# Optimization experiments

Measured on AMD Instinct MI355X. Metric: run time of the kernel, lower is better.

The kernel has to match this reference:

```python
import jax, jax.numpy as jnp
import numpy as np

BIT = 64
N_DATA = 200000
TOP_FNPS = 20
THRESHOLD = 0.3
K = 2500
T = 0.9 * float(np.sqrt(BIT))
MOMENTUM = 0.4
HIGH = int(N_DATA * 0.9)
BATCH = 256


def _l2norm(x):
    return x / jnp.linalg.norm(x, axis=-1, keepdims=True)


def setup_inputs() -> dict:
    key = jax.random.key(0)
    ks = jax.random.split(key, 7)
    i_A = jax.random.normal(ks[0], (BATCH, BIT), jnp.float32)
    i_B = jax.random.normal(ks[1], (BATCH, BIT), jnp.float32)
    t_A = jax.random.normal(ks[2], (BATCH, BIT), jnp.float32)
    t_B = jax.random.normal(ks[3], (BATCH, BIT), jnp.float32)
    # memory bank: F.normalize(sign(randn)) -> rows are +-1/sqrt(bit)
    memory = jnp.sign(jax.random.normal(ks[4], (N_DATA, BIT), jnp.float32)) / np.float32(np.sqrt(BIT))
    # uniform keys used for randperm-equivalent negative sampling (top-K of random keys)
    rand_u = jax.random.uniform(ks[5], (BATCH, N_DATA), jnp.float32)
    batch_idx = jax.random.randint(ks[6], (BATCH,), 0, N_DATA)
    return {"i_A": i_A, "i_B": i_B, "t_A": t_A, "t_B": t_B,
            "memory": memory, "rand_u": rand_u, "batch_idx": batch_idx}


def reference(i_A, i_B, t_A, t_B, memory, rand_u, batch_idx):
    f1 = (i_A + t_A) * 0.5  # anchor fusion [B, bit]
    f2 = (i_A + t_B) * 0.5
    f3 = (i_B + t_A) * 0.5
    f4 = (i_B + t_B) * 0.5
    # sim_k = memory @ norm(f_k).T ; final_sim = mean of 4 (mm is linear in the fusion)
    fsum = (_l2norm(f1) + _l2norm(f2) + _l2norm(f3) + _l2norm(f4)) * 0.25
    final_sim = fsum @ memory.T  # [B, N]

    def per_sample(sim_col, ru, pos, anchor):
        # sim_col: [N], ru: [N] uniform keys, pos: scalar idx, anchor: [bit]
        topv, topi = jax.lax.top_k(sim_col, TOP_FNPS)
        fnp_valid = (topv > THRESHOLD) & (topi != pos)  # false-negative pairs mask
        excl = jnp.zeros((N_DATA,), bool).at[topi].set(fnp_valid).at[pos].set(True)
        # candidates = top HIGH entries of descending sort == sims >= HIGH-th largest value
        kth = jnp.sort(sim_col)[N_DATA - HIGH]
        cand = (sim_col >= kth) & (~excl)
        keys = jnp.where(cand, ru, -jnp.inf)
        _, neg_idx = jax.lax.top_k(keys, K)  # uniform K-subset of candidates
        pos_s = jnp.sign(memory[pos])          # [bit]
        fnp_s = jnp.sign(memory[topi])         # [TOP_FNPS, bit]
        neg_s = jnp.sign(memory[neg_idx])      # [K, bit]
        pos_sim = jnp.dot(pos_s, anchor) / T
        fnp_sim = (fnp_s @ anchor) / T
        neg_sim = (neg_s @ anchor) / T
        vmask = fnp_valid.astype(anchor.dtype)
        pos_exp = jnp.exp(pos_sim)
        # numerator = pos_exp + sum(beta * fnp_exp), beta = fnp_sim
        numerator = pos_exp + jnp.sum(fnp_sim * jnp.exp(fnp_sim) * vmask)
        denominator = jnp.sum(jnp.exp(neg_sim)) + pos_exp
        n_fnp = jnp.sum(vmask)
        return -jnp.log(numerator / denominator) / (1.0 + n_fnp)

    losses = jax.vmap(per_sample)(final_sim, rand_u, batch_idx, f1)
    avg_loss = jnp.mean(losses)

    # momentum memory-bank update (torch.no_grad block)
    new_feature = _l2norm(f1)
    old_feature = memory[batch_idx] * MOMENTUM + new_feature * (1.0 - MOMENTUM)
    old_feature = _l2norm(old_feature)
    new_memory = memory.at[batch_idx].set(old_feature)
    return avg_loss, new_memory
```

## Files before the change

kernel.cpp:

```cpp
#include <hip/hip_runtime.h>
#include <stdint.h>

#define NDATA 200000
#define BATCH 256
#define BITD  64
#define TOPF  20
#define KNEG  2500
#define RANKA 20000
#define TVAL  7.2f
#define S8T   (8.0f/7.2f)
#define THRV  0.3f
#define TAU   0.983f
#define KHINV 60235.294f

#define NB    512
#define HCUT  320
#define HLO   (-0.35f)
#define HINV  1024.0f

#define CFX   2048
#define CNX3  4096
#define NCHK  200
#define CAPN  44
#define CAPF  36
#define WCH   8
#define BLKF  512
#define HSLC  8

typedef unsigned long long u64;
typedef __attribute__((ext_vector_type(16))) float f32x16;
typedef __attribute__((ext_vector_type(8))) short s16x8;

__device__ __forceinline__ int binOf(float sim) {
    int b = (int)floorf((sim - HLO) * HINV);
    b = b < 0 ? 0 : b;
    b = b > (NB - 1) ? (NB - 1) : b;
    return b;
}
__device__ __forceinline__ unsigned short bf16_rne(float x) {
    unsigned u = __float_as_uint(x);
    unsigned r = (u + 0x7FFFu + ((u >> 16) & 1u)) >> 16;
    return (unsigned short)r;
}
__device__ __forceinline__ float bf2f(unsigned short u) {
    return __uint_as_float(((unsigned)u) << 16);
}

__global__ __launch_bounds__(64) void k_prep(
    const float* __restrict__ iA, const float* __restrict__ iB,
    const float* __restrict__ tA, const float* __restrict__ tB,
    const float* __restrict__ mem, const int* __restrict__ bidx,
    unsigned short* __restrict__ fsumHi, unsigned short* __restrict__ fsumLo,
    float* __restrict__ fsumF, float* __restrict__ f1_g,
    float* __restrict__ upd_g, float* __restrict__ posExp_g,
    unsigned* __restrict__ hist_gp,
    unsigned* __restrict__ negBaseG, unsigned* __restrict__ fnpBaseG)
{
    int s = blockIdx.x, j = threadIdx.x;
    float a = iA[s * BITD + j], b = iB[s * BITD + j];
    float c = tA[s * BITD + j], d = tB[s * BITD + j];
    float f1 = 0.5f * (a + c), f2 = 0.5f * (a + d);
    float f3 = 0.5f * (b + c), f4 = 0.5f * (b + d);
    float q1 = f1 * f1, q2 = f2 * f2, q3 = f3 * f3, q4 = f4 * f4;
#pragma unroll
    for (int m = 1; m < 64; m <<= 1) {
        q1 += __shfl_xor(q1, m); q2 += __shfl_xor(q2, m);
        q3 += __shfl_xor(q3, m); q4 += __shfl_xor(q4, m);
    }
    float n1 = sqrtf(q1), n2 = sqrtf(q2), n3 = sqrtf(q3), n4 = sqrtf(q4);
    float fs = 0.25f * (f1 / n1 + f2 / n2 + f3 / n3 + f4 / n4);

    unsigned short hi = bf16_rne(fs);
    float hif = __uint_as_float(((unsigned)hi) << 16);
    unsigned short lo = bf16_rne(fs - hif);
    fsumHi[s * BITD + j] = hi;
    fsumLo[s * BITD + j] = lo;
    fsumF[s * BITD + j] = fs;
    f1_g[s * BITD + j] = f1;

    int pos = bidx[s];
    float mv = mem[(size_t)pos * BITD + j];
    float sg = (mv > 0.f) ? 1.f : ((mv < 0.f) ? -1.f : 0.f);
    float ps = sg * f1;
#pragma unroll
    for (int m = 1; m < 64; m <<= 1) ps += __shfl_xor(ps, m);

    float nf = f1 / n1;
    float u = mv * 0.4f + nf * 0.6f;
    float uq = u * u;
#pragma unroll
    for (int m = 1; m < 64; m <<= 1) uq += __shfl_xor(uq, m);
    upd_g[s * BITD + j] = u / sqrtf(uq);

    if (j == 0) {
        posExp_g[s] = expf(ps / TVAL);
        negBaseG[s] = 0u; fnpBaseG[s] = 0u;
    }
    int gtid = s * 64 + j;
    for (int k = gtid; k < HSLC * (BATCH / 2) * HCUT; k += BATCH * 64) hist_gp[k] = 0u;
}

__global__ __launch_bounds__(256) void k_pack(const float* __restrict__ mem,
                                              unsigned short* __restrict__ memB,
                                              float* __restrict__ out)
{
    int t2 = blockIdx.x;
    int t = threadIdx.x;
    int sl = t & 31, h = (t >> 5) & 1, ks = t >> 6;
    int row = t2 * 32 + sl;
    int col = ks * 16 + 8 * h;
    const float* src = mem + (size_t)row * BITD + col;
    float4 v0 = *(const float4*)src;
    float4 v1 = *(const float4*)(src + 4);
    s16x8 o;
    o[0] = (short)bf16_rne(v0.x); o[1] = (short)bf16_rne(v0.y);
    o[2] = (short)bf16_rne(v0.z); o[3] = (short)bf16_rne(v0.w);
    o[4] = (short)bf16_rne(v1.x); o[5] = (short)bf16_rne(v1.y);
    o[6] = (short)bf16_rne(v1.z); o[7] = (short)bf16_rne(v1.w);
    *(s16x8*)(memB + ((size_t)(t2 * 4 + ks) * 2 + h) * 256 + sl * 8) = o;
    float* dst = out + 1 + (size_t)row * BITD + col;
    dst[0] = v0.x; dst[1] = v0.y; dst[2] = v0.z; dst[3] = v0.w;
    dst[4] = v1.x; dst[5] = v1.y; dst[6] = v1.z; dst[7] = v1.w;
}

__global__ __launch_bounds__(256, 4) void k_main(
    const unsigned short* __restrict__ memB, const float* __restrict__ ru,
    const unsigned short* __restrict__ fsumHi, const unsigned short* __restrict__ fsumLo,
    const float* __restrict__ f1_g, const float* __restrict__ fsumF,
    unsigned* __restrict__ negPayC, u64* __restrict__ fnpPayC,
    unsigned* __restrict__ negBaseG, unsigned* __restrict__ fnpBaseG,
    unsigned* __restrict__ hist_gp)
{
    __shared__ unsigned histL[8 * HCUT];
    __shared__ unsigned negPayL[32 * CAPN * 3];
    __shared__ u64 fnpPayL[32 * CAPF];
    __shared__ unsigned negCntL[32], fnpCntL[32];
    __shared__ unsigned negBaseL[32], fnpBaseL[32];

    const int tid = threadIdx.x;
    const int w = tid >> 6, l = tid & 63;
    const int h = l >> 5, sl = l & 31;

    const int bid = blockIdx.x;
    const int chunk = (bid & 7) + 8 * (bid >> 6);
    const int smpblk = (bid >> 3) & 7;
    const int slice = bid & 7;
    const int sbBase = smpblk * 32;
    const int chunkBase = chunk * 1024;
    if (chunkBase >= NDATA) return;

    for (int q = tid; q < 8 * HCUT; q += 256) histL[q] = 0u;
    if (tid < 32) { negCntL[tid] = 0u; fnpCntL[tid] = 0u; }
    __syncthreads();

    s16x8 aHi[4], aLo[4];
    {
        const unsigned short* ph = fsumHi + (size_t)(sbBase + sl) * BITD + 8 * h;
        const unsigned short* pl = fsumLo + (size_t)(sbBase + sl) * BITD + 8 * h;
#pragma unroll
        for (int ks = 0; ks < 4; ++ks) {
            aHi[ks] = *(const s16x8*)(ph + ks * 16);
            aLo[ks] = *(const s16x8*)(pl + ks * 16);
        }
    }
    const s16x8* bp = (const s16x8*)memB;

    s16x8 bcur[4], bnxt[4];
    {
        int waveRow = chunkBase + 32 * w;
        int t2 = (waveRow < NDATA) ? (waveRow >> 5) : 0;
#pragma unroll
        for (int ks = 0; ks < 4; ++ks)
            bcur[ks] = bp[((size_t)(t2 * 4 + ks) * 2 + h) * 32 + sl];
    }

    for (int it = 0; it < WCH; ++it) {
        const int waveRow = chunkBase + it * 128 + 32 * w;
        const bool valid = (waveRow < NDATA);

        {
            int nRow = chunkBase + (it + 1) * 128 + 32 * w;
            int t2 = (it + 1 < WCH && nRow < NDATA) ? (nRow >> 5) : 0;
#pragma unroll
            for (int ks = 0; ks < 4; ++ks)
                bnxt[ks] = bp[((size_t)(t2 * 4 + ks) * 2 + h) * 32 + sl];
        }

        if (valid) {
            f32x16 acc;
#pragma unroll
            for (int i = 0; i < 16; ++i) acc[i] = 0.f;
#pragma unroll
            for (int ks = 0; ks < 4; ++ks) {
                acc = __builtin_amdgcn_mfma_f32_32x32x16_bf16(aHi[ks], bcur[ks], acc, 0, 0, 0);
                acc = __builtin_amdgcn_mfma_f32_32x32x16_bf16(aLo[ks], bcur[ks], acc, 0, 0, 0);
            }

            const int grow = waveRow + sl;
#pragma unroll
            for (int i = 0; i < 16; ++i) {
                float sim = acc[i];
                int smpL = (i & 3) + 8 * (i >> 2) + 4 * h;
                int bin = binOf(sim);
                if (bin < HCUT)
                    atomicAdd(&histL[(smpL >> 2) * HCUT + bin], 1u << (8 * (i & 3)));

                bool pf = sim > THRV;
                u64 mF = __ballot(pf);
                unsigned halfF = (unsigned)(mF >> (h << 5));
                if (halfF) {
                    unsigned baseF = 0;
                    if (sl == 0) baseF = atomicAdd(&fnpCntL[smpL], __popc(halfF));
                    baseF = __shfl(baseF, h << 5);
                    if (pf) {
                        unsigned slot = baseF + __popc(halfF & ((1u << sl) - 1u));
                        if (slot < CAPF)
                            fnpPayL[smpL * CAPF + slot] =
                                ((u64)__float_as_uint(sim) << 32) | (u64)(0x3FFFFu - (unsigned)grow);
                    }
                }
            }
        }
#pragma unroll
        for (int ks = 0; ks < 4; ++ks) bcur[ks] = bnxt[ks];
    }

    {
        int rbase = chunkBase + tid * 4;
        if (rbase < NDATA) {
            for (int smp = 0; smp < 32; ++smp) {
                float4 kv = *(const float4*)&ru[(size_t)(sbBase + smp) * NDATA + rbase];
                const float kvv[4] = {kv.x, kv.y, kv.z, kv.w};
#pragma unroll
                for (int k = 0; k < 4; ++k) {
                    if (kvv[k] > TAU) {
                        unsigned slot = atomicAdd(&negCntL[smp], 1u);
                        if (slot < CAPN) {
                            negPayL[(smp * CAPN + slot) * 3] = 0x3FFFFu - (unsigned)(rbase + k);
                            negPayL[(smp * CAPN + slot) * 3 + 1] = __float_as_uint(kvv[k]);
                        }
                    }
                }
            }
        }
    }
    __syncthreads();

    {
        const int smp = tid >> 3, sub = tid & 7;
        const float* fsp = fsumF + (size_t)(sbBase + smp) * BITD + sub * 8;
        const float* f1p = f1_g + (size_t)(sbBase + smp) * BITD + sub * 8;
        float4 fs0 = ((const float4*)fsp)[0], fs1 = ((const float4*)fsp)[1];
        float4 f10 = ((const float4*)f1p)[0], f11 = ((const float4*)f1p)[1];
        const float fsr[8] = {fs0.x, fs0.y, fs0.z, fs0.w, fs1.x, fs1.y, fs1.z, fs1.w};
        const float f1r[8] = {f10.x, f10.y, f10.z, f10.w, f11.x, f11.y, f11.z, f11.w};
        unsigned cnt = negCntL[smp]; if (cnt > CAPN) cnt = CAPN;
        for (int e = 0; e < (int)cnt; ++e) {
            unsigned w0 = negPayL[(smp * CAPN + e) * 3];
            unsigned row = 0x3FFFFu - (w0 & 0x3FFFFu);
            s16x8 v = bp[((size_t)((row >> 5) * 4 + (sub >> 1)) * 2 + (sub & 1)) * 32 + (row & 31)];
            float ev = 0.f, sv = 0.f;
#pragma unroll
            for (int k = 0; k < 8; ++k) {
                float f = bf2f((unsigned short)v[k]);
                ev = fmaf(f, f1r[k], ev);
                sv = fmaf(f, fsr[k], sv);
            }
#pragma unroll
            for (int off = 1; off < 8; off <<= 1) {
                ev += __shfl_xor(ev, off);
                sv += __shfl_xor(sv, off);
            }
            if (sub == 0) {
                negPayL[(smp * CAPN + e) * 3] = w0 | ((unsigned)binOf(sv) << 18);
                negPayL[(smp * CAPN + e) * 3 + 2] = __float_as_uint(ev);
            }
        }
    }
    __syncthreads();

    if (tid < 32) {
        unsigned cn2 = negCntL[tid]; if (cn2 > CAPN) cn2 = CAPN;
        negBaseL[tid] = atomicAdd(&negBaseG[sbBase + tid], cn2);
        unsigned cf2 = fnpCntL[tid]; if (cf2 > CAPF) cf2 = CAPF;
        fnpBaseL[tid] = atomicAdd(&fnpBaseG[sbBase + tid], cf2);
    }
    __syncthreads();
    for (int q = tid; q < 32 * CAPN * 3; q += 256) {
        int smp = q / (CAPN * 3), r = q % (CAPN * 3);
        unsigned cnt = negCntL[smp]; if (cnt > CAPN) cnt = CAPN;
        if (r < (int)cnt * 3) {
            unsigned e = negBaseL[smp] + (unsigned)(r / 3);
            if (e < CNX3)
                negPayC[((size_t)(sbBase + smp) * CNX3 + e) * 3 + (r % 3)] =
                    negPayL[smp * (CAPN * 3) + r];
        }
    }
    for (int q = tid; q < 32 * CAPF; q += 256) {
        int smp = q / CAPF, r = q % CAPF;
        unsigned cf2 = fnpCntL[smp]; if (cf2 > CAPF) cf2 = CAPF;
        if (r < (int)cf2) {
            unsigned e = fnpBaseL[smp] + (unsigned)r;
            if (e < CFX)
                fnpPayC[(size_t)(sbBase + smp) * CFX + e] = fnpPayL[q];
        }
    }
    for (int g = 0; g < 8; ++g) {
        for (int bin = tid; bin < HCUT; bin += 256) {
            unsigned wv = histL[g * HCUT + bin];
            if (!wv) continue;
            unsigned c0 = wv & 0xffu, c1 = (wv >> 8) & 0xffu;
            unsigned c2 = (wv >> 16) & 0xffu, c3 = wv >> 24;
            int sBase = sbBase + g * 4;
            unsigned p01 = c0 | (c1 << 16), p23 = c2 | (c3 << 16);
            size_t sb = (size_t)slice * (BATCH / 2);
            if (p01) atomicAdd(&hist_gp[(sb + (sBase >> 1)) * HCUT + bin], p01);
            if (p23) atomicAdd(&hist_gp[(sb + (sBase >> 1) + 1) * HCUT + bin], p23);
        }
    }
}

__global__ __launch_bounds__(BLKF, 1) void k_fin(
    const int* __restrict__ bidx,
    const unsigned* __restrict__ negPayC, const u64* __restrict__ fnpPayC,
    const unsigned* __restrict__ negBaseG, const unsigned* __restrict__ fnpBaseG,
    const unsigned* __restrict__ hist_gp, const float* __restrict__ posExp_g,
    const float* __restrict__ f1_g, const unsigned short* __restrict__ memB,
    float* __restrict__ losses)
{
    __shared__ u64 arrF[CFX];
    __shared__ unsigned payL[CNX3 * 3];
    __shared__ unsigned khist[1024];
    __shared__ unsigned scr[HCUT];
    __shared__ float redF[BLKF];
    __shared__ u64 wtop[8 * TOPF];
    __shared__ u64 winPk[TOPF];
    __shared__ unsigned exclR[TOPF];
    __shared__ float numW[TOPF];
    __shared__ u64 bndV[64];
    __shared__ float bndE[64];
    __shared__ float f1sh[BITD];
    __shared__ int shI[4];
    __shared__ float shNum;
    __shared__ unsigned bndCnt;

    const int s = blockIdx.x, tid = threadIdx.x;
    const int w8 = tid >> 6, l = tid & 63;
    const int pos = bidx[s];
    const s16x8* bp = (const s16x8*)memB;

    if (tid == 0) bndCnt = 0u;
    if (tid < 16) ((float4*)f1sh)[tid] = ((const float4*)&f1_g[(size_t)s * BITD])[tid];
    if (tid < HCUT) {
        int sh = (s & 1) * 16;
        unsigned acc = 0;
#pragma unroll
        for (int sl2 = 0; sl2 < HSLC; ++sl2)
            acc += (hist_gp[((size_t)sl2 * (BATCH / 2) + (s >> 1)) * HCUT + tid] >> sh) & 0xffffu;
        scr[tid] = acc;
    }
    khist[tid] = 0u; khist[tid + BLKF] = 0u;

    unsigned cn = negBaseG[s]; if (cn > CNX3) cn = CNX3;
    unsigned cf = fnpBaseG[s]; if (cf > CFX) cf = CFX;
    for (int q = tid; q < (int)cn * 3; q += BLKF)
        payL[q] = negPayC[(size_t)s * CNX3 * 3 + q];
    for (int i = tid; i < CFX; i += BLKF)
        arrF[i] = (i < (int)cf) ? fnpPayC[(size_t)s * CFX + i] : 0ull;
    __syncthreads();

    if (tid == 0) {
        unsigned cum = 0; int beta = HCUT - 1;
        for (int b2 = 0; b2 < HCUT; ++b2) {
            cum += scr[b2];
            if (cum >= (unsigned)(RANKA + 1)) { beta = b2; break; }
        }
        shI[0] = beta;
    }

    {
        u64 ta[4];
#pragma unroll
        for (int j = 0; j < 4; ++j) ta[j] = arrF[tid + j * BLKF];
#pragma unroll
        for (int k = 0; k < TOPF; ++k) {
            u64 m = ta[0];
#pragma unroll
            for (int j = 1; j < 4; ++j) if (ta[j] > m) m = ta[j];
#pragma unroll
            for (int off = 1; off < 64; off <<= 1) { u64 o = __shfl_xor(m, off); if (o > m) m = o; }
            if (l == 0) wtop[w8 * TOPF + k] = m;
#pragma unroll
            for (int j = 0; j < 4; ++j) if (ta[j] == m) ta[j] = 0ull;
        }
    }
    __syncthreads();
    if (w8 == 0) {
        u64 t0 = (l < 8 * TOPF) ? wtop[l] : 0ull;
        u64 t1 = (l + 64 < 8 * TOPF) ? wtop[l + 64] : 0ull;
        u64 t2 = (l + 128 < 8 * TOPF) ? wtop[l + 128] : 0ull;
#pragma unroll
        for (int k = 0; k < TOPF; ++k) {
            u64 m = t0;
            if (t1 > m) m = t1;
            if (t2 > m) m = t2;
#pragma unroll
            for (int off = 1; off < 64; off <<= 1) { u64 o = __shfl_xor(m, off); if (o > m) m = o; }
            if (l == 0) winPk[k] = m;
            if (t0 == m) t0 = 0ull;
            if (t1 == m) t1 = 0ull;
            if (t2 == m) t2 = 0ull;
        }
    }
    __syncthreads();
    if (tid == 0) {
        int ne = 0;
        for (int wi = 0; wi < TOPF; ++wi) {
            u64 pk = winPk[wi];
            if (pk == 0ull) break;
            unsigned row = 0x3FFFFu - (unsigned)(pk & 0x3FFFFull);
            if ((int)row != pos) exclR[ne++] = row;
        }
        shI[1] = ne;
    }
    __syncthreads();
    const int beta = shI[0], ne = shI[1];

    {
        int grp = tid >> 2, lp = tid & 3;
        if (grp < ne) {
            unsigned row = exclR[grp];
            int blk2 = (int)(row >> 5), sl2 = (int)(row & 31);
            float part = 0.f;
#pragma unroll
            for (int h2 = 0; h2 < 2; ++h2) {
                s16x8 v = bp[((size_t)(blk2 * 4 + lp) * 2 + h2) * 32 + sl2];
#pragma unroll
                for (int k = 0; k < 8; ++k)
                    part = fmaf(bf2f((unsigned short)v[k]), f1sh[lp * 16 + 8 * h2 + k], part);
            }
            part += __shfl_xor(part, 1);
            part += __shfl_xor(part, 2);
            if (lp == 0) {
                float fsim = part * S8T;
                numW[grp] = fsim * expf(fsim);
            }
        }
    }
    __syncthreads();
    if (tid == 0) {
        float numer = posExp_g[s];
        for (int g = 0; g < ne; ++g) numer += numW[g];
        shNum = numer;
    }
    __syncthreads();

    for (int i = tid; i < (int)cn; i += BLKF) {
        unsigned w0 = payL[i * 3];
        unsigned row = 0x3FFFFu - (w0 & 0x3FFFFu);
        int bin = (int)(w0 >> 18);
        if ((int)row == pos || bin < beta) continue;
        bool ex = false;
        for (int q2 = 0; q2 < ne; ++q2) ex = ex || (exclR[q2] == row);
        if (ex) continue;
        float key = __uint_as_float(payL[i * 3 + 1]);
        int kb = (int)((key - TAU) * KHINV);
        kb = kb < 0 ? 0 : (kb > 1023 ? 1023 : kb);
        atomicAdd(&khist[kb], 1u);
    }
    __syncthreads();
    if (tid == 0) {
        unsigned acc2 = 0; int Bs = 0;
        for (int b2 = 1023; b2 >= 0; --b2) {
            unsigned c2 = khist[b2];
            if (acc2 + c2 >= (unsigned)KNEG) { Bs = b2; break; }
            acc2 += c2;
            if (b2 == 0) Bs = 0;
        }
        shI[2] = Bs;
        shI[3] = (int)acc2;
    }
    __syncthreads();
    const int Bstar = shI[2];

    float dsum = 0.f;
    for (int i = tid; i < (int)cn; i += BLKF) {
        unsigned w0 = payL[i * 3];
        unsigned row = 0x3FFFFu - (w0 & 0x3FFFFu);
        int bin = (int)(w0 >> 18);
        if ((int)row == pos || bin < beta) continue;
        bool ex = false;
        for (int q2 = 0; q2 < ne; ++q2) ex = ex || (exclR[q2] == row);
        if (ex) continue;
        float key = __uint_as_float(payL[i * 3 + 1]);
        int kb = (int)((key - TAU) * KHINV);
        kb = kb < 0 ? 0 : (kb > 1023 ? 1023 : kb);
        if (kb > Bstar) {
            dsum += expf(__uint_as_float(payL[i * 3 + 2]) * S8T);
        } else if (kb == Bstar) {
            unsigned sl3 = atomicAdd(&bndCnt, 1u);
            if (sl3 < 64u) {
                bndV[sl3] = ((u64)__float_as_uint(key) << 32) | (u64)(0x3FFFFu - row);
                bndE[sl3] = __uint_as_float(payL[i * 3 + 2]);
            }
        }
    }
    redF[tid] = dsum;
    __syncthreads();
    for (int st = BLKF / 2; st > 0; st >>= 1) {
        if (tid < st) redF[tid] += redF[tid + st];
        __syncthreads();
    }
    if (tid == 0) {
        int C1 = shI[3];
        int m = KNEG - C1;
        int bc = (int)bndCnt; if (bc > 64) bc = 64;
        if (m > bc) m = bc;
        if (m < 0) m = 0;
        float bsum = 0.f;
        for (int t2 = 0; t2 < m; ++t2) {
            u64 best = 0; int bi = -1;
            for (int q2 = 0; q2 < bc; ++q2)
                if (bndV[q2] > best) { best = bndV[q2]; bi = q2; }
            bsum += expf(bndE[bi] * S8T);
            bndV[bi] = 0;
        }
        float D = redF[0] + bsum + posExp_g[s];
        losses[s] = -logf(shNum / D) / (1.0f + (float)ne);
    }
}

__global__ __launch_bounds__(256) void k_loss(const float* __restrict__ losses,
                                              float* __restrict__ out)
{
    __shared__ float buf[256];
    int t = threadIdx.x;
    buf[t] = losses[t];
    __syncthreads();
    for (int st = 128; st > 0; st >>= 1) {
        if (t < st) buf[t] += buf[t + st];
        __syncthreads();
    }
    if (t == 0) out[0] = buf[0] / 256.0f;
}

__global__ __launch_bounds__(64) void k_scatter(const int* __restrict__ bidx,
                                                const float* __restrict__ upd,
                                                float* __restrict__ out)
{
    int s = blockIdx.x, j = threadIdx.x;
    int pos = bidx[s];
    bool last = true;
    for (int s2 = s + 1; s2 < BATCH; ++s2)
        if (bidx[s2] == pos) last = false;
    if (last) out[1 + (size_t)pos * BITD + j] = upd[s * BITD + j];
}

extern "C" void kernel_launch(void* const* d_in, const int* in_sizes, int n_in,
                              void* d_out, int out_size, void* d_ws, size_t ws_size,
                              hipStream_t stream)
{
    const float* iA = (const float*)d_in[0];
    const float* iB = (const float*)d_in[1];
    const float* tA = (const float*)d_in[2];
    const float* tB = (const float*)d_in[3];
    const float* mem = (const float*)d_in[4];
    const float* ru  = (const float*)d_in[5];
    const int* bidx  = (const int*)d_in[6];
    float* out = (float*)d_out;

    char* w = (char*)d_ws;
    unsigned* negPayC = (unsigned*)w;  w += (size_t)BATCH * CNX3 * 3 * 4;
    u64* fnpPayC = (u64*)w;            w += (size_t)BATCH * CFX * 8;
    unsigned short* memB = (unsigned short*)w; w += (size_t)NDATA * BITD * 2;
    unsigned* negBaseG = (unsigned*)w; w += BATCH * 4;
    unsigned* fnpBaseG = (unsigned*)w; w += BATCH * 4;
    unsigned* hist_gp = (unsigned*)w;  w += (size_t)HSLC * (BATCH / 2) * HCUT * 4;
    float* fsumF = (float*)w;          w += BATCH * BITD * 4;
    float* f1_g = (float*)w;           w += BATCH * BITD * 4;
    float* upd_g = (float*)w;          w += BATCH * BITD * 4;
    float* posExp_g = (float*)w;       w += BATCH * 4;
    float* losses = (float*)w;         w += BATCH * 4;
    unsigned short* fsumHi = (unsigned short*)w; w += BATCH * BITD * 2;
    unsigned short* fsumLo = (unsigned short*)w; w += BATCH * BITD * 2;

    k_prep<<<BATCH, 64, 0, stream>>>(iA, iB, tA, tB, mem, bidx, fsumHi, fsumLo,
                                     fsumF, f1_g, upd_g, posExp_g, hist_gp,
                                     negBaseG, fnpBaseG);
    k_pack<<<NDATA / 32, 256, 0, stream>>>(mem, memB, out);
    k_main<<<NCHK * 8, 256, 0, stream>>>(memB, ru, fsumHi, fsumLo, f1_g, fsumF,
                                         negPayC, fnpPayC, negBaseG, fnpBaseG, hist_gp);
    k_fin<<<BATCH, BLKF, 0, stream>>>(bidx, negPayC, fnpPayC, negBaseG, fnpBaseG,
                                      hist_gp, posExp_g, f1_g, memB, losses);
    k_loss<<<1, 256, 0, stream>>>(losses, out);
    k_scatter<<<BATCH, 64, 0, stream>>>(bidx, upd_g, out);
}
```

Before: 286.3 us.

## Split negative sampling out of k_main into separate k_neg kernel

Moves the random-key scan and negative-candidate payload generation into a new k_neg kernel, leaving k_main with only the MFMA similarity, histogram and false-negative collection. Each kernel then needs less LDS and fewer registers, so k_main's launch bounds rise from 4 to 8 blocks per CU and k_neg runs at 6. The FNP slot allocation also drops the wave ballot in favour of a per-lane LDS atomic. The cost is an extra kernel launch and no overlap between the memory-bound ru scan and the MFMA work.

```diff
diff --git a/kernel.cpp b/kernel.cpp
--- a/kernel.cpp
+++ b/kernel.cpp
@@ -123,19 +123,15 @@
     dst[4] = v1.x; dst[5] = v1.y; dst[6] = v1.z; dst[7] = v1.w;
 }
 
-__global__ __launch_bounds__(256, 4) void k_main(
-    const unsigned short* __restrict__ memB, const float* __restrict__ ru,
+__global__ __launch_bounds__(256, 8) void k_main(
+    const unsigned short* __restrict__ memB,
     const unsigned short* __restrict__ fsumHi, const unsigned short* __restrict__ fsumLo,
-    const float* __restrict__ f1_g, const float* __restrict__ fsumF,
-    unsigned* __restrict__ negPayC, u64* __restrict__ fnpPayC,
-    unsigned* __restrict__ negBaseG, unsigned* __restrict__ fnpBaseG,
+    u64* __restrict__ fnpPayC, unsigned* __restrict__ fnpBaseG,
     unsigned* __restrict__ hist_gp)
 {
     __shared__ unsigned histL[8 * HCUT];
-    __shared__ unsigned negPayL[32 * CAPN * 3];
     __shared__ u64 fnpPayL[32 * CAPF];
-    __shared__ unsigned negCntL[32], fnpCntL[32];
-    __shared__ unsigned negBaseL[32], fnpBaseL[32];
+    __shared__ unsigned fnpCntL[32], fnpBaseL[32];
 
     const int tid = threadIdx.x;
     const int w = tid >> 6, l = tid & 63;
@@ -150,7 +146,7 @@
     if (chunkBase >= NDATA) return;
 
     for (int q = tid; q < 8 * HCUT; q += 256) histL[q] = 0u;
-    if (tid < 32) { negCntL[tid] = 0u; fnpCntL[tid] = 0u; }
+    if (tid < 32) fnpCntL[tid] = 0u;
     __syncthreads();
 
     s16x8 aHi[4], aLo[4];
@@ -204,26 +200,67 @@
                 int bin = binOf(sim);
                 if (bin < HCUT)
                     atomicAdd(&histL[(smpL >> 2) * HCUT + bin], 1u << (8 * (i & 3)));
-
-                bool pf = sim > THRV;
-                u64 mF = __ballot(pf);
-                unsigned halfF = (unsigned)(mF >> (h << 5));
-                if (halfF) {
-                    unsigned baseF = 0;
-                    if (sl == 0) baseF = atomicAdd(&fnpCntL[smpL], __popc(halfF));
-                    baseF = __shfl(baseF, h << 5);
-                    if (pf) {
-                        unsigned slot = baseF + __popc(halfF & ((1u << sl) - 1u));
-                        if (slot < CAPF)
-                            fnpPayL[smpL * CAPF + slot] =
-                                ((u64)__float_as_uint(sim) << 32) | (u64)(0x3FFFFu - (unsigned)grow);
-                    }
+                if (sim > THRV) {
+                    unsigned slot = atomicAdd(&fnpCntL[smpL], 1u);
+                    if (slot < CAPF)
+                        fnpPayL[smpL * CAPF + slot] =
+                            ((u64)__float_as_uint(sim) << 32) | (u64)(0x3FFFFu - (unsigned)grow);
                 }
             }
         }
 #pragma unroll
         for (int ks = 0; ks < 4; ++ks) bcur[ks] = bnxt[ks];
     }
+    __syncthreads();
+
+    if (tid < 32) {
+        unsigned cf2 = fnpCntL[tid]; if (cf2 > CAPF) cf2 = CAPF;
+        fnpBaseL[tid] = atomicAdd(&fnpBaseG[sbBase + tid], cf2);
+    }
+    __syncthreads();
+    for (int q = tid; q < 32 * CAPF; q += 256) {
+        int smp = q / CAPF, r = q % CAPF;
+        unsigned cf2 = fnpCntL[smp]; if (cf2 > CAPF) cf2 = CAPF;
+        if (r < (int)cf2) {
+            unsigned e = fnpBaseL[smp] + (unsigned)r;
+            if (e < CFX)
+                fnpPayC[(size_t)(sbBase + smp) * CFX + e] = fnpPayL[q];
+        }
+    }
+    for (int g = 0; g < 8; ++g) {
+        for (int bin = tid; bin < HCUT; bin += 256) {
+            unsigned wv = histL[g * HCUT + bin];
+            if (!wv) continue;
+            unsigned c0 = wv & 0xffu, c1 = (wv >> 8) & 0xffu;
+            unsigned c2 = (wv >> 16) & 0xffu, c3 = wv >> 24;
+            int sBase = sbBase + g * 4;
+            unsigned p01 = c0 | (c1 << 16), p23 = c2 | (c3 << 16);
+            size_t sb = (size_t)slice * (BATCH / 2);
+            if (p01) atomicAdd(&hist_gp[(sb + (sBase >> 1)) * HCUT + bin], p01);
+            if (p23) atomicAdd(&hist_gp[(sb + (sBase >> 1) + 1) * HCUT + bin], p23);
+        }
+    }
+}
+
+__global__ __launch_bounds__(256, 6) void k_neg(
+    const unsigned short* __restrict__ memB, const float* __restrict__ ru,
+    const float* __restrict__ f1_g, const float* __restrict__ fsumF,
+    unsigned* __restrict__ negPayC, unsigned* __restrict__ negBaseG)
+{
+    __shared__ unsigned negPayL[32 * CAPN * 3];
+    __shared__ unsigned negCntL[32], negBaseL[32];
+
+    const int tid = threadIdx.x;
+    const int bid = blockIdx.x;
+    const int chunk = (bid & 7) + 8 * (bid >> 6);
+    const int smpblk = (bid >> 3) & 7;
+    const int sbBase = smpblk * 32;
+    const int chunkBase = chunk * 1024;
+    if (chunkBase >= NDATA) return;
+
+    if (tid < 32) negCntL[tid] = 0u;
+    __syncthreads();
+    const s16x8* bp = (const s16x8*)memB;
 
     {
         int rbase = chunkBase + tid * 4;
@@ -282,8 +319,6 @@
     if (tid < 32) {
         unsigned cn2 = negCntL[tid]; if (cn2 > CAPN) cn2 = CAPN;
         negBaseL[tid] = atomicAdd(&negBaseG[sbBase + tid], cn2);
-        unsigned cf2 = fnpCntL[tid]; if (cf2 > CAPF) cf2 = CAPF;
-        fnpBaseL[tid] = atomicAdd(&fnpBaseG[sbBase + tid], cf2);
     }
     __syncthreads();
     for (int q = tid; q < 32 * CAPN * 3; q += 256) {
@@ -294,28 +329,6 @@
             if (e < CNX3)
                 negPayC[((size_t)(sbBase + smp) * CNX3 + e) * 3 + (r % 3)] =
                     negPayL[smp * (CAPN * 3) + r];
-        }
-    }
-    for (int q = tid; q < 32 * CAPF; q += 256) {
-        int smp = q / CAPF, r = q % CAPF;
-        unsigned cf2 = fnpCntL[smp]; if (cf2 > CAPF) cf2 = CAPF;
-        if (r < (int)cf2) {
-            unsigned e = fnpBaseL[smp] + (unsigned)r;
-            if (e < CFX)
-                fnpPayC[(size_t)(sbBase + smp) * CFX + e] = fnpPayL[q];
-        }
-    }
-    for (int g = 0; g < 8; ++g) {
-        for (int bin = tid; bin < HCUT; bin += 256) {
-            unsigned wv = histL[g * HCUT + bin];
-            if (!wv) continue;
-            unsigned c0 = wv & 0xffu, c1 = (wv >> 8) & 0xffu;
-            unsigned c2 = (wv >> 16) & 0xffu, c3 = wv >> 24;
-            int sBase = sbBase + g * 4;
-            unsigned p01 = c0 | (c1 << 16), p23 = c2 | (c3 << 16);
-            size_t sb = (size_t)slice * (BATCH / 2);
-            if (p01) atomicAdd(&hist_gp[(sb + (sBase >> 1)) * HCUT + bin], p01);
-            if (p23) atomicAdd(&hist_gp[(sb + (sBase >> 1) + 1) * HCUT + bin], p23);
         }
     }
 }
@@ -588,8 +601,9 @@
                                      fsumF, f1_g, upd_g, posExp_g, hist_gp,
                                      negBaseG, fnpBaseG);
     k_pack<<<NDATA / 32, 256, 0, stream>>>(mem, memB, out);
-    k_main<<<NCHK * 8, 256, 0, stream>>>(memB, ru, fsumHi, fsumLo, f1_g, fsumF,
-                                         negPayC, fnpPayC, negBaseG, fnpBaseG, hist_gp);
+    k_main<<<NCHK * 8, 256, 0, stream>>>(memB, fsumHi, fsumLo,
+                                         fnpPayC, fnpBaseG, hist_gp);
+    k_neg<<<NCHK * 8, 256, 0, stream>>>(memB, ru, f1_g, fsumF, negPayC, negBaseG);
     k_fin<<<BATCH, BLKF, 0, stream>>>(bidx, negPayC, fnpPayC, negBaseG, fnpBaseG,
                                       hist_gp, posExp_g, f1_g, memB, losses);
     k_loss<<<1, 256, 0, stream>>>(losses, out);
```

After: 342.4 us. +19.6%, slower.
